# Kernel tuning notes

Measured on AMD Instinct MI355X. Metric: run time of the kernel, lower is better.

Reference implementation:

```python
import jax, jax.numpy as jnp
import numpy as np

HEADS = 8


def setup_inputs() -> dict:
    key = jax.random.key(0)
    ks = jax.random.split(key, 12)
    B, H, W, C = 2, 128, 256, 256
    inner = C  # num_heads * dim_head = 8 * 32

    def p(k, shape):
        return jax.random.normal(k, shape, dtype=jnp.float32) * 0.02

    return {
        "x": jax.random.normal(ks[0], (B, H * W, C), dtype=jnp.float32),
        "Wq_h": p(ks[1], (C, inner)),
        "Wk_h": p(ks[2], (C, inner)),
        "Wv_h": p(ks[3], (C, inner)),
        "Wo_h": p(ks[4], (inner, C)),
        "bo_h": p(ks[5], (C,)),
        "Wq_w": p(ks[6], (C, inner)),
        "Wk_w": p(ks[7], (C, inner)),
        "Wv_w": p(ks[8], (C, inner)),
        "Wo_w": p(ks[9], (inner, C)),
        "bo_w": p(ks[10], (C,)),
        "h": H,
        "w": W,
    }


def reference(x, Wq_h, Wk_h, Wv_h, Wo_h, bo_h, Wq_w, Wk_w, Wv_w, Wo_w, bo_w, h, w):
    b, n, c = x.shape
    heads = HEADS
    d = Wq_h.shape[1] // heads  # dim_head
    scale = d ** -0.5
    xs = x.reshape(b, h, w, c)  # [B,H,W,C]

    def proj(Wm):
        # [B,H,W,heads,d]
        return (xs @ Wm).reshape(b, h, w, heads, d)

    # --- height-axis attention: each column attends across all rows ---
    q, k, v = proj(Wq_h), proj(Wk_h), proj(Wv_h)
    s = jnp.einsum('bxwnd,bywnd->bwnxy', q, k) * scale  # [B,W,heads,H,H]
    a = jax.nn.softmax(s, axis=-1)
    oh = jnp.einsum('bwnxy,bywnd->bxwnd', a, v).reshape(b, h, w, heads * d)
    oh = oh @ Wo_h + bo_h

    # --- width-axis attention: each row attends across all columns ---
    q, k, v = proj(Wq_w), proj(Wk_w), proj(Wv_w)
    s = jnp.einsum('bhxnd,bhynd->bhnxy', q, k) * scale  # [B,H,heads,W,W]
    a = jax.nn.softmax(s, axis=-1)
    ow = jnp.einsum('bhnxy,bhynd->bhxnd', a, v).reshape(b, h, w, heads * d)
    ow = ow @ Wo_w + bo_w

    return (oh + ow).reshape(b, n, c)
```

## Files before the change

kernel.cpp:

```cpp
#include <hip/hip_runtime.h>
#include <hip/hip_bf16.h>
#include <stdint.h>

typedef unsigned short u16;
typedef short bf16x8 __attribute__((ext_vector_type(8)));
typedef float f32x4  __attribute__((ext_vector_type(4)));
typedef float f32x16 __attribute__((ext_vector_type(16)));
typedef unsigned int u32x4 __attribute__((ext_vector_type(4)));

__device__ __forceinline__ u16 f2bf(float f) {
    uint32_t u = __builtin_bit_cast(uint32_t, f);
    u += 0x7fffu + ((u >> 16) & 1u);
    return (u16)(u >> 16);
}

#if __has_builtin(__builtin_amdgcn_exp2f)
#define EXP2(x) __builtin_amdgcn_exp2f(x)
#else
extern "C" __device__ float __ocml_native_exp2_f32(float);
#define EXP2(x) __ocml_native_exp2_f32(x)
#endif

__device__ __forceinline__ void gl_lds16(const u16* g, u16* l) {
    __builtin_amdgcn_global_load_lds(
        (__attribute__((address_space(1))) void*)(g),
        (__attribute__((address_space(3))) void*)(l),
        16, 0, 0);
}

#define MM 65536
#define CC 256

#define QSCALE (1.4426950408889634f * 0.17677669529663687f)

__device__ __forceinline__ int perm_h(int t) {
    return ((t >> 15) << 15) | ((t & 127) << 8) | ((t >> 7) & 255);
}


__global__ void prep_kernel(
    const float* __restrict__ Wq_h, const float* __restrict__ Wk_h, const float* __restrict__ Wv_h,
    const float* __restrict__ Wo_h, const float* __restrict__ bo_h,
    const float* __restrict__ Wq_w, const float* __restrict__ Wk_w, const float* __restrict__ Wv_w,
    const float* __restrict__ Wo_w, const float* __restrict__ bo_w,
    u16* __restrict__ Wh_t, u16* __restrict__ Ww_t,
    u16* __restrict__ Woh_t, u16* __restrict__ Wow_t,
    u16* __restrict__ Wocat, float* __restrict__ bias)
{
    const int tid = blockIdx.x * 256 + threadIdx.x;
    const int nth = gridDim.x * 256;

    for (int i = tid; i < 768 * 256; i += nth) {
        int n = i >> 8, kk = i & 255;
        int which = n >> 8, nn = n & 255;
        const float* Wsh = (which == 0) ? Wq_h : (which == 1) ? Wk_h : Wv_h;
        const float* Wsw = (which == 0) ? Wq_w : (which == 1) ? Wk_w : Wv_w;
        Wh_t[i] = f2bf(Wsh[kk * 256 + nn]);
        Ww_t[i] = f2bf(Wsw[kk * 256 + nn]);
    }
    for (int i = tid; i < 256 * 256; i += nth) {
        int n = i >> 8, k = i & 255;
        Woh_t[i] = f2bf(Wo_h[k * 256 + n]);
        Wow_t[i] = f2bf(Wo_w[k * 256 + n]);
    }
    for (int i = tid; i < 256 * 512; i += nth) {
        int n = i >> 9, k = i & 511;
        float v = (k < 256) ? Wo_h[k * 256 + n] : Wo_w[(k - 256) * 256 + n];
        Wocat[i] = f2bf(v);
    }
    for (int i = tid; i < 256; i += nth) bias[i] = bo_h[i] + bo_w[i];
}

__global__ __launch_bounds__(256) void xcvt_kernel(const float* __restrict__ x, u16* __restrict__ xb)
{
    int i = blockIdx.x * 256 + threadIdx.x;
    const int nth = gridDim.x * 256;
    const int total = MM * 256 / 8;
    for (; i < total; i += nth) {
        const float* ap = x + (size_t)i * 8;
        float4 f0 = *(const float4*)ap;
        float4 f1 = *(const float4*)(ap + 4);
        u16 o[8] = { f2bf(f0.x), f2bf(f0.y), f2bf(f0.z), f2bf(f0.w),
                     f2bf(f1.x), f2bf(f1.y), f2bf(f1.z), f2bf(f1.w) };
        *(int4*)(xb + (size_t)i * 8) = *(const int4*)o;
    }
}

template<int PH>
__global__ __launch_bounds__(512) void gemm_qkv_kernel(
    const u16* __restrict__ xb, const u16* __restrict__ Bt,
    u16* __restrict__ Qb, u16* __restrict__ Kb, u16* __restrict__ Vb)
{
    constexpr int S = PH ? 128 : 256;
    constexpr int L = PH ? 7 : 8;
    const int K = 256;
    __shared__ u16 sh[24576];
    u16* As = sh;
    u16* Bs = sh + 16384;
    const int tid = threadIdx.x;
    const int lane = tid & 63, wave = tid >> 6;
    const int wm = wave >> 1, wn = wave & 1;
    const int l15 = lane & 15, lq = lane >> 4;

    const int id = blockIdx.x;
    const int xcd = id & 7, wq = id >> 3;
    const int mt = xcd * 32 + wq / 6, nt = wq % 6;
    const int m0 = mt * 256, n0 = nt * 128;

    f32x4 acc[4][4];
#pragma unroll
    for (int i = 0; i < 4; i++)
#pragma unroll
        for (int j = 0; j < 4; j++)
#pragma unroll
            for (int t = 0; t < 4; t++) acc[i][j][t] = 0.0f;

    for (int kt = 0; kt < K; kt += 64) {
        __syncthreads();
#pragma unroll
        for (int i = 0; i < 4; i++) {
            int cid = i * 512 + tid;
            int r = cid >> 3, sc = cid & 7;
            int gk = kt + ((sc ^ (r & 7)) << 3);
            int rm = PH ? perm_h(m0 + r) : (m0 + r);
            gl_lds16(xb + (size_t)rm * 256 + gk, As + cid * 8);
        }
#pragma unroll
        for (int i = 0; i < 2; i++) {
            int cid = i * 512 + tid;
            int r = cid >> 3, sc = cid & 7;
            int gk = kt + ((sc ^ (r & 7)) << 3);
            gl_lds16(Bt + (size_t)(n0 + r) * K + gk, Bs + cid * 8);
        }
        __syncthreads();
#pragma unroll
        for (int ks = 0; ks < 2; ks++) {
            bf16x8 af[4], bfr[4];
#pragma unroll
            for (int i = 0; i < 4; i++) {
                int row = wm * 64 + i * 16 + l15;
                int ca  = ks * 4 + lq;
                af[i]  = *(const bf16x8*)(As + row * 64 + ((ca ^ (row & 7)) << 3));
                int nn  = wn * 64 + i * 16 + l15;
                bfr[i] = *(const bf16x8*)(Bs + nn * 64 + ((ca ^ (nn & 7)) << 3));
            }
#pragma unroll
            for (int i = 0; i < 4; i++)
#pragma unroll
                for (int j = 0; j < 4; j++)
                    acc[i][j] = __builtin_amdgcn_mfma_f32_16x16x32_bf16(af[i], bfr[j], acc[i][j], 0, 0, 0);
        }
    }

    const int ln_ = lane & 31, lh_ = lane >> 5;

    if (nt < 4) {
        const float scale = (nt < 2) ? (float)QSCALE : 1.0f;
        u16* dstb = (nt < 2) ? Qb : Kb;
        const int hg = wave & 3;
        const int half = wave >> 2;
        const int head = (nt & 1) * 4 + hg;

#pragma unroll
        for (int p = 0; p < 2; p++) {
            __syncthreads();
            if ((wm >> 1) == p) {
#pragma unroll
                for (int i = 0; i < 4; i++)
#pragma unroll
                    for (int j = 0; j < 4; j++)
#pragma unroll
                        for (int r = 0; r < 4; r++) {
                            int row = (wm & 1) * 64 + i * 16 + lq * 4 + r;
                            int col = wn * 64 + j * 16 + l15;
                            sh[row * 128 + (col ^ ((row & 7) << 3))] = f2bf(acc[i][j][r] * scale);
                        }
            }
            __syncthreads();
            int base = m0 + p * 128;
            int gi = base >> L;
            int seqbase = base & (S - 1);
            u16* dst = dstb + ((size_t)(gi * 8 + head) * S + seqbase) * 32;
#pragma unroll
            for (int qt = 0; qt < 4; qt++) {
                int row  = qt * 32 + ln_;
                int colb = hg * 32 + half * 16 + lh_ * 8;
                int4 v = *(const int4*)(sh + row * 128 + (colb ^ ((row & 7) << 3)));
                *(int4*)(dst + qt * 1024 + half * 512 + lane * 8) = v;
            }
        }
    } else {
        const int hh = wave & 3;
        const int tq = wave >> 2;
        const int head = (nt - 4) * 4 + hh;

#pragma unroll
        for (int p = 0; p < 2; p++) {
            __syncthreads();
            if ((wm >> 1) == p) {
#pragma unroll
                for (int i = 0; i < 4; i++)
#pragma unroll
                    for (int j = 0; j < 4; j++)
#pragma unroll
                        for (int r = 0; r < 4; r++) {
                            int row = (wm & 1) * 64 + i * 16 + lq * 4 + r;
                            int col = wn * 64 + j * 16 + l15;
                            sh[row * 128 + (col ^ ((row & 7) << 3))] = f2bf(acc[i][j][r]);
                        }
            }
            __syncthreads();
            int base = m0 + p * 128;
            int gi = base >> L;
            int seqbase = base & (S - 1);
            u16* dst = Vb + ((size_t)(gi * 8 + head) * S + seqbase) * 32;
#pragma unroll
            for (int tt = 0; tt < 2; tt++) {
                int t = tq * 2 + tt;
#pragma unroll
                for (int half = 0; half < 2; half++) {
                    u16 o[8];
#pragma unroll
                    for (int j = 0; j < 8; j++) {
                        int row = t * 32 + half * 16 + lh_ * 8 + j;
                        int col = hh * 32 + ln_;
                        o[j] = sh[row * 128 + (col ^ ((row & 7) << 3))];
                    }
                    *(int4*)(dst + t * 1024 + half * 512 + lane * 8) = *(const int4*)o;
                }
            }
        }
    }
}

template<int PH>
__global__ __launch_bounds__(512) void gemm_qk_kernel(
    const float* __restrict__ x, const u16* __restrict__ Bt,
    u16* __restrict__ Qb, u16* __restrict__ Kb)
{
    constexpr int S = PH ? 128 : 256;
    constexpr int L = PH ? 7 : 8;
    const int K = 256;
    __shared__ u16 sh[24576];
    u16* As = sh;
    u16* Bs = sh + 16384;
    const int tid = threadIdx.x;
    const int lane = tid & 63, wave = tid >> 6;
    const int wm = wave >> 1, wn = wave & 1;
    const int l15 = lane & 15, lq = lane >> 4;

    const int id = blockIdx.x;
    const int xcd = id & 7, wq = id >> 3;
    const int mt = xcd * 32 + (wq >> 2), nt = wq & 3;
    const int m0 = mt * 256, n0 = nt * 128;

    f32x4 acc[4][4];
#pragma unroll
    for (int i = 0; i < 4; i++)
#pragma unroll
        for (int j = 0; j < 4; j++)
#pragma unroll
            for (int t = 0; t < 4; t++) acc[i][j][t] = 0.0f;

    for (int kt = 0; kt < K; kt += 64) {
        __syncthreads();
#pragma unroll
        for (int i = 0; i < 4; i++) {
            int cid = i * 512 + tid;
            int r = cid >> 3, sc = cid & 7;
            int gk = kt + ((sc ^ (r & 7)) << 3);
            int rm = PH ? perm_h(m0 + r) : (m0 + r);
            const float* ap = x + (size_t)rm * 256 + gk;
            float4 f0 = *(const float4*)ap;
            float4 f1 = *(const float4*)(ap + 4);
            u16 o[8] = { f2bf(f0.x), f2bf(f0.y), f2bf(f0.z), f2bf(f0.w),
                         f2bf(f1.x), f2bf(f1.y), f2bf(f1.z), f2bf(f1.w) };
            *(int4*)(As + (size_t)cid * 8) = *(const int4*)o;
        }
#pragma unroll
        for (int i = 0; i < 2; i++) {
            int cid = i * 512 + tid;
            int r = cid >> 3, sc = cid & 7;
            int gk = kt + ((sc ^ (r & 7)) << 3);
            *(int4*)(Bs + (size_t)cid * 8) = *(const int4*)(Bt + (size_t)(n0 + r) * K + gk);
        }
        __syncthreads();
#pragma unroll
        for (int ks = 0; ks < 2; ks++) {
            bf16x8 af[4], bfr[4];
#pragma unroll
            for (int i = 0; i < 4; i++) {
                int row = wm * 64 + i * 16 + l15;
                int ca  = ks * 4 + lq;
                af[i]  = *(const bf16x8*)(As + row * 64 + ((ca ^ (row & 7)) << 3));
                int nn  = wn * 64 + i * 16 + l15;
                bfr[i] = *(const bf16x8*)(Bs + nn * 64 + ((ca ^ (nn & 7)) << 3));
            }
#pragma unroll
            for (int i = 0; i < 4; i++)
#pragma unroll
                for (int j = 0; j < 4; j++)
                    acc[i][j] = __builtin_amdgcn_mfma_f32_16x16x32_bf16(af[i], bfr[j], acc[i][j], 0, 0, 0);
        }
    }

    const float scale = (nt < 2) ? (float)QSCALE : 1.0f;
    u16* dstb = (nt < 2) ? Qb : Kb;
    const int ln_ = lane & 31, lh_ = lane >> 5;
    const int hg = wave & 3;
    const int half = wave >> 2;
    const int head = (nt & 1) * 4 + hg;

#pragma unroll
    for (int p = 0; p < 2; p++) {
        __syncthreads();
        if ((wm >> 1) == p) {
#pragma unroll
            for (int i = 0; i < 4; i++)
#pragma unroll
                for (int j = 0; j < 4; j++)
#pragma unroll
                    for (int r = 0; r < 4; r++) {
                        int row = (wm & 1) * 64 + i * 16 + lq * 4 + r;
                        int col = wn * 64 + j * 16 + l15;
                        sh[row * 128 + (col ^ ((row & 7) << 3))] = f2bf(acc[i][j][r] * scale);
                    }
        }
        __syncthreads();
        int base = m0 + p * 128;
        int gi = base >> L;
        int seqbase = base & (S - 1);
        u16* dst = dstb + ((size_t)(gi * 8 + head) * S + seqbase) * 32;
#pragma unroll
        for (int qt = 0; qt < 4; qt++) {
            int row  = qt * 32 + ln_;
            int colb = hg * 32 + half * 16 + lh_ * 8;
            int4 v = *(const int4*)(sh + row * 128 + (colb ^ ((row & 7) << 3)));
            *(int4*)(dst + qt * 1024 + half * 512 + lane * 8) = v;
        }
    }
}

template<int PH>
__global__ __launch_bounds__(256) void gemm_vt_kernel(
    const u16* __restrict__ Wt, const float* __restrict__ x, u16* __restrict__ Vb)
{
    constexpr int S = PH ? 128 : 256;
    const int K = 256;
    __shared__ u16 sh[16384];
    u16* As = sh;
    u16* Bs = sh + 8192;
    const int tid = threadIdx.x;
    const int lane = tid & 63, wave = tid >> 6;
    const int wm = wave & 1, wn = wave >> 1;
    const int l15 = lane & 15, lq = lane >> 4;
    const int m0 = blockIdx.y * 128, n0 = blockIdx.x * 128;

    f32x4 acc[4][4];
#pragma unroll
    for (int i = 0; i < 4; i++)
#pragma unroll
        for (int j = 0; j < 4; j++)
#pragma unroll
            for (int t = 0; t < 4; t++) acc[i][j][t] = 0.0f;

    for (int kt = 0; kt < K; kt += 64) {
        __syncthreads();
#pragma unroll
        for (int i = 0; i < 4; i++) {
            int cid = i * 256 + tid;
            int r = cid >> 3, sc = cid & 7;
            int gk = kt + ((sc ^ (r & 7)) << 3);
            *(int4*)(As + (size_t)cid * 8) = *(const int4*)(Wt + (size_t)(m0 + r) * K + gk);
            int cm = PH ? perm_h(n0 + r) : (n0 + r);
            const float* bp = x + (size_t)cm * 256 + gk;
            float4 f0 = *(const float4*)bp;
            float4 f1 = *(const float4*)(bp + 4);
            u16 o[8] = { f2bf(f0.x), f2bf(f0.y), f2bf(f0.z), f2bf(f0.w),
                         f2bf(f1.x), f2bf(f1.y), f2bf(f1.z), f2bf(f1.w) };
            *(int4*)(Bs + (size_t)cid * 8) = *(const int4*)o;
        }
        __syncthreads();
#pragma unroll
        for (int ks = 0; ks < 2; ks++) {
            bf16x8 af[4], bfr[4];
#pragma unroll
            for (int i = 0; i < 4; i++) {
                int row = wm * 64 + i * 16 + l15;
                int ca  = ks * 4 + lq;
                af[i]  = *(const bf16x8*)(As + row * 64 + ((ca ^ (row & 7)) << 3));
                int nn  = wn * 64 + i * 16 + l15;
                bfr[i] = *(const bf16x8*)(Bs + nn * 64 + ((ca ^ (nn & 7)) << 3));
            }
#pragma unroll
            for (int i = 0; i < 4; i++)
#pragma unroll
                for (int j = 0; j < 4; j++)
                    acc[i][j] = __builtin_amdgcn_mfma_f32_16x16x32_bf16(af[i], bfr[j], acc[i][j], 0, 0, 0);
        }
    }

    __syncthreads();
#pragma unroll
    for (int i = 0; i < 4; i++)
#pragma unroll
        for (int j = 0; j < 4; j++)
#pragma unroll
            for (int r = 0; r < 4; r++) {
                int row = wm * 64 + i * 16 + lq * 4 + r;
                int col = wn * 64 + j * 16 + l15;
                sh[row * 128 + (col ^ ((row & 7) << 3))] = f2bf(acc[i][j][r]);
            }
    __syncthreads();

    const int gi = n0 >> (PH ? 7 : 8);
    const int seqbase = n0 & (S - 1);
    const int head = (m0 >> 5) + wave;
    u16* dst = Vb + ((size_t)(gi * 8 + head) * S + seqbase) * 32;
    const int ln_ = lane & 31, lh_ = lane >> 5;
#pragma unroll
    for (int cl = 0; cl < 4; cl++)
#pragma unroll
        for (int half = 0; half < 2; half++) {
            int row  = wave * 32 + ln_;
            int colb = cl * 32 + half * 16 + lh_ * 8;
            int4 v = *(const int4*)(sh + row * 128 + (colb ^ ((row & 7) << 3)));
            *(int4*)(dst + cl * 1024 + half * 512 + lane * 8) = v;
        }
}

__global__ __launch_bounds__(512) void gemm_out_fused_kernel(
    const u16* __restrict__ Ah, const u16* __restrict__ Aw,
    const u16* __restrict__ Bcat, float* __restrict__ Cout, const float* __restrict__ bias)
{
    const int K = 512, N = 256;
    __shared__ u16 sh[24576];
    u16* As = sh;
    u16* Bs = sh + 16384;
    const int tid = threadIdx.x;
    const int lane = tid & 63, wave = tid >> 6;
    const int wm = wave >> 1, wn = wave & 1;
    const int l15 = lane & 15, lq = lane >> 4;

    const int id = blockIdx.x;
    const int xcd = id & 7, wq = id >> 3;
    const int mt = xcd * 32 + (wq >> 1), nt = wq & 1;
    const int m0 = mt * 256, n0 = nt * 128;

    f32x4 acc[4][4];
#pragma unroll
    for (int i = 0; i < 4; i++)
#pragma unroll
        for (int j = 0; j < 4; j++)
#pragma unroll
            for (int t = 0; t < 4; t++) acc[i][j][t] = 0.0f;

    for (int kt = 0; kt < K; kt += 64) {
        __syncthreads();
        const u16* Abase = (kt < 256) ? Ah : Aw;
        int koff = kt & 255;
#pragma unroll
        for (int i = 0; i < 4; i++) {
            int cid = i * 512 + tid;
            int r = cid >> 3, sc = cid & 7;
            int gs = (sc ^ (r & 7)) << 3;
            gl_lds16(Abase + (size_t)(m0 + r) * 256 + koff + gs, As + cid * 8);
        }
#pragma unroll
        for (int i = 0; i < 2; i++) {
            int cid = i * 512 + tid;
            int r = cid >> 3, sc = cid & 7;
            int gs = (sc ^ (r & 7)) << 3;
            gl_lds16(Bcat + (size_t)(n0 + r) * K + kt + gs, Bs + cid * 8);
        }
        __syncthreads();
#pragma unroll
        for (int ks = 0; ks < 2; ks++) {
            bf16x8 af[4], bfr[4];
#pragma unroll
            for (int i = 0; i < 4; i++) {
                int row = wm * 64 + i * 16 + l15;
                int ca  = ks * 4 + lq;
                af[i]  = *(const bf16x8*)(As + row * 64 + ((ca ^ (row & 7)) << 3));
                int nn  = wn * 64 + i * 16 + l15;
                bfr[i] = *(const bf16x8*)(Bs + nn * 64 + ((ca ^ (nn & 7)) << 3));
            }
#pragma unroll
            for (int i = 0; i < 4; i++)
#pragma unroll
                for (int j = 0; j < 4; j++)
                    acc[i][j] = __builtin_amdgcn_mfma_f32_16x16x32_bf16(af[i], bfr[j], acc[i][j], 0, 0, 0);
        }
    }
#pragma unroll
    for (int i = 0; i < 4; i++)
#pragma unroll
        for (int j = 0; j < 4; j++)
#pragma unroll
            for (int r = 0; r < 4; r++) {
                int row = m0 + wm * 64 + i * 16 + lq * 4 + r;
                int col = n0 + wn * 64 + j * 16 + l15;
                Cout[(size_t)row * N + col] = acc[i][j][r] + bias[col];
            }
}

template<int MODE>
__global__ __launch_bounds__(256) void gemm_out_kernel(
    const u16* __restrict__ A16, const u16* __restrict__ Bt,
    float* __restrict__ Cout, const float* __restrict__ bias)
{
    const int K = 256, N = 256;
    __shared__ u16 As[128 * 64];
    __shared__ u16 Bs[128 * 64];
    const int tid = threadIdx.x;
    const int lane = tid & 63, wave = tid >> 6;
    const int wm = wave & 1, wn = wave >> 1;
    const int l15 = lane & 15, lq = lane >> 4;
    const int m0 = blockIdx.y * 128, n0 = blockIdx.x * 128;

    f32x4 acc[4][4];
#pragma unroll
    for (int i = 0; i < 4; i++)
#pragma unroll
        for (int j = 0; j < 4; j++)
#pragma unroll
            for (int t = 0; t < 4; t++) acc[i][j][t] = 0.0f;

    for (int kt = 0; kt < K; kt += 64) {
        __syncthreads();
#pragma unroll
        for (int i = 0; i < 4; i++) {
            int cid = i * 256 + tid;
            int r = cid >> 3, sc = cid & 7;
            int gk = kt + ((sc ^ (r & 7)) << 3);
            *(int4*)(As + (size_t)cid * 8) = *(const int4*)(A16 + (size_t)(m0 + r) * K + gk);
            *(int4*)(Bs + (size_t)cid * 8) = *(const int4*)(Bt + (size_t)(n0 + r) * K + gk);
        }
        __syncthreads();
#pragma unroll
        for (int ks = 0; ks < 2; ks++) {
            bf16x8 af[4], bfr[4];
#pragma unroll
            for (int i = 0; i < 4; i++) {
                int row = wm * 64 + i * 16 + l15;
                int ca  = ks * 4 + lq;
                af[i]  = *(const bf16x8*)(As + row * 64 + ((ca ^ (row & 7)) << 3));
                int nn  = wn * 64 + i * 16 + l15;
                bfr[i] = *(const bf16x8*)(Bs + nn * 64 + ((ca ^ (nn & 7)) << 3));
            }
#pragma unroll
            for (int i = 0; i < 4; i++)
#pragma unroll
                for (int j = 0; j < 4; j++)
                    acc[i][j] = __builtin_amdgcn_mfma_f32_16x16x32_bf16(af[i], bfr[j], acc[i][j], 0, 0, 0);
        }
    }
#pragma unroll
    for (int i = 0; i < 4; i++)
#pragma unroll
        for (int j = 0; j < 4; j++)
#pragma unroll
            for (int r = 0; r < 4; r++) {
                int row = m0 + wm * 64 + i * 16 + lq * 4 + r;
                int col = n0 + wn * 64 + j * 16 + l15;
                size_t idx = (size_t)row * N + col;
                if (MODE == 1) Cout[idx] = acc[i][j][r] + bias[col];
                else           Cout[idx] += acc[i][j][r];
            }
}

template<int S, int PH, int NT>
__global__ __launch_bounds__(NT) void attn_kernel(
    const u16* __restrict__ Qb, const u16* __restrict__ Kb,
    const u16* __restrict__ Vb, u16* __restrict__ att)
{
    constexpr int NC = S / 32;
    const int tid = threadIdx.x;
    const int lane = tid & 63;
    const int wave = tid >> 6;
    const int ln = lane & 31;
    const int lh = lane >> 5;

    const int bid = blockIdx.x;
    const int head = bid & 7;
    const int gi = bid >> 3;
    const int qs = wave * 32;
    const int g = gi * 8 + head;

    const u16* Qg = Qb + (size_t)g * S * 32;
    const u16* Kg = Kb + (size_t)g * S * 32;
    const u16* Vg = Vb + (size_t)g * S * 32;

    const u16* qp = Qg + (qs >> 5) * 1024 + lane * 8;
    bf16x8 bq0 = *(const bf16x8*)qp;
    bf16x8 bq1 = *(const bf16x8*)(qp + 512);

    f32x16 kz;
#pragma unroll
    for (int t = 0; t < 16; t++) kz[t] = 0.0f;
    asm("" : "+v"(kz));

    float rs[4] = {0.0f, 0.0f, 0.0f, 0.0f};
    f32x16 oacc;
#pragma unroll
    for (int t = 0; t < 16; t++) oacc[t] = 0.0f;

    const u16* kp0 = Kg + lane * 8;
    const u16* vp0 = Vg + lane * 8;
    bf16x8 ak0 = *(const bf16x8*)kp0;
    bf16x8 ak1 = *(const bf16x8*)(kp0 + 512);
    bf16x8 bv0 = *(const bf16x8*)vp0;
    bf16x8 bv1 = *(const bf16x8*)(vp0 + 512);

    for (int c = 0; c < NC; c++) {
        f32x16 z = __builtin_amdgcn_mfma_f32_32x32x16_bf16(ak0, bq0, kz, 0, 0, 0);
        z = __builtin_amdgcn_mfma_f32_32x32x16_bf16(ak1, bq1, z, 0, 0, 0);

        int cn = (c + 1 < NC) ? c + 1 : c;
        const u16* kp = kp0 + cn * 1024;
        const u16* vp = vp0 + cn * 1024;
        bf16x8 nk0 = *(const bf16x8*)kp;
        bf16x8 nk1 = *(const bf16x8*)(kp + 512);
        bf16x8 nv0 = *(const bf16x8*)vp;
        bf16x8 nv1 = *(const bf16x8*)(vp + 512);

        asm("" : "+v"(z));
        float p[16];
#pragma unroll
        for (int r = 0; r < 16; r++) { p[r] = EXP2(z[r]); rs[r & 3] += p[r]; }

        unsigned w[8];
#pragma unroll
        for (int t = 0; t < 8; t++) {
            unsigned d;
            asm("v_cvt_pk_bf16_f32 %0, %1, %2" : "=v"(d) : "v"(p[2 * t]), "v"(p[2 * t + 1]));
            w[t] = d;
        }
        auto s0 = __builtin_amdgcn_permlane32_swap(w[0], w[2], false, false);
        auto s1 = __builtin_amdgcn_permlane32_swap(w[1], w[3], false, false);
        auto s2 = __builtin_amdgcn_permlane32_swap(w[4], w[6], false, false);
        auto s3 = __builtin_amdgcn_permlane32_swap(w[5], w[7], false, false);
        u32x4 a0 = { (unsigned)s0[0], (unsigned)s1[0], (unsigned)s0[1], (unsigned)s1[1] };
        u32x4 a1 = { (unsigned)s2[0], (unsigned)s3[0], (unsigned)s2[1], (unsigned)s3[1] };
        bf16x8 pa0 = __builtin_bit_cast(bf16x8, a0);
        bf16x8 pa1 = __builtin_bit_cast(bf16x8, a1);

        oacc = __builtin_amdgcn_mfma_f32_32x32x16_bf16(pa0, bv0, oacc, 0, 0, 0);
        oacc = __builtin_amdgcn_mfma_f32_32x32x16_bf16(pa1, bv1, oacc, 0, 0, 0);

        ak0 = nk0; ak1 = nk1; bv0 = nv0; bv1 = nv1;
    }

    float rsum = (rs[0] + rs[1]) + (rs[2] + rs[3]);
    rsum += __shfl_xor(rsum, 32);
    float inv = 1.0f / rsum;
#pragma unroll
    for (int r = 0; r < 16; r++) {
        int row = (r & 3) + ((r >> 2) << 3) + (lh << 2);
        float is = __shfl(inv, row);
        int seq = qs + row;
        int m = PH ? ((gi >> 8) * 32768 + seq * 256 + (gi & 255))
                   : (gi * 256 + seq);
        att[(size_t)m * 256 + head * 32 + ln] = f2bf(oacc[r] * is);
    }
}

extern "C" void kernel_launch(void* const* d_in, const int* in_sizes, int n_in,
                              void* d_out, int out_size, void* d_ws, size_t ws_size,
                              hipStream_t stream)
{
    (void)in_sizes; (void)n_in; (void)out_size;
    const float* x    = (const float*)d_in[0];
    const float* Wq_h = (const float*)d_in[1];
    const float* Wk_h = (const float*)d_in[2];
    const float* Wv_h = (const float*)d_in[3];
    const float* Wo_h = (const float*)d_in[4];
    const float* bo_h = (const float*)d_in[5];
    const float* Wq_w = (const float*)d_in[6];
    const float* Wk_w = (const float*)d_in[7];
    const float* Wv_w = (const float*)d_in[8];
    const float* Wo_w = (const float*)d_in[9];
    const float* bo_w = (const float*)d_in[10];

    const size_t NB = (size_t)MM * 256;
    u16* Qb   = (u16*)d_ws;
    u16* Kb   = Qb + NB;
    u16* Vb   = Kb + NB;
    u16* attb = Vb + NB;
    u16* xb   = attb + NB;
    const size_t WT = (size_t)2 * 768 * 256 + (size_t)2 * 256 * 256 + (size_t)256 * 512 + 512;
    const bool use_xb = ws_size >= (5 * NB + WT) * sizeof(u16);
    u16* wp = use_xb ? (xb + NB) : xb;
    u16* Wh_t  = wp;
    u16* Ww_t  = Wh_t + 768 * 256;
    u16* Woh_t = Ww_t + 768 * 256;
    u16* Wow_t = Woh_t + 256 * 256;
    u16* Wocat = Wow_t + 256 * 256;
    float* bias = (float*)(Wocat + 256 * 512);

    prep_kernel<<<512, 256, 0, stream>>>(Wq_h, Wk_h, Wv_h, Wo_h, bo_h,
                                         Wq_w, Wk_w, Wv_w, Wo_w, bo_w,
                                         Wh_t, Ww_t, Woh_t, Wow_t, Wocat, bias);
    if (use_xb)
        xcvt_kernel<<<8192, 256, 0, stream>>>(x, xb);

    if (use_xb) {
        gemm_qkv_kernel<1><<<1536, 512, 0, stream>>>(xb, Wh_t, Qb, Kb, Vb);
        attn_kernel<128, 1, 256><<<4096, 256, 0, stream>>>(Qb, Kb, Vb, attb);

        gemm_qkv_kernel<0><<<1536, 512, 0, stream>>>(xb, Ww_t, Qb, Kb, Vb);
        attn_kernel<256, 0, 512><<<2048, 512, 0, stream>>>(Qb, Kb, Vb, xb);

        gemm_out_fused_kernel<<<512, 512, 0, stream>>>(attb, xb, Wocat,
                                                       (float*)d_out, bias);
    } else {
        gemm_qk_kernel<1><<<1024, 512, 0, stream>>>(x, Wh_t, Qb, Kb);
        gemm_vt_kernel<1><<<dim3(512, 2), 256, 0, stream>>>(Wh_t + 512 * 256, x, Vb);
        attn_kernel<128, 1, 256><<<4096, 256, 0, stream>>>(Qb, Kb, Vb, attb);
        gemm_out_kernel<1><<<dim3(2, 512), 256, 0, stream>>>(attb, Woh_t, (float*)d_out, bias);

        gemm_qk_kernel<0><<<1024, 512, 0, stream>>>(x, Ww_t, Qb, Kb);
        gemm_vt_kernel<0><<<dim3(512, 2), 256, 0, stream>>>(Ww_t + 512 * 256, x, Vb);
        attn_kernel<256, 0, 512><<<2048, 512, 0, stream>>>(Qb, Kb, Vb, attb);
        gemm_out_kernel<2><<<dim3(2, 512), 256, 0, stream>>>(attb, Wow_t, (float*)d_out, nullptr);
    }
}
```

Baseline: 337.9 us.

## Merge height and width QKV and attention passes into single launches

Folds the x-to-bf16 conversion into the weight prep kernel. When the workspace is large enough, it also keeps separate Q/K/V buffers for the two axes, so both QKV GEMMs run in one launch and both attention passes run in one launch. This removes launch gaps and tail effects from serial kernels and gives larger grids for better occupancy. In exchange it needs more workspace, and the code falls back to the old path if the workspace is too small.

Measured after the change: 335.7 us. About the same (-0.6%).

```diff
diff --git a/kernel.cpp b/kernel.cpp
--- a/kernel.cpp
+++ b/kernel.cpp
@@ -38,14 +38,15 @@
 }
 
 
-__global__ void prep_kernel(
+__global__ __launch_bounds__(256) void prepx_kernel(
     const float* __restrict__ Wq_h, const float* __restrict__ Wk_h, const float* __restrict__ Wv_h,
     const float* __restrict__ Wo_h, const float* __restrict__ bo_h,
     const float* __restrict__ Wq_w, const float* __restrict__ Wk_w, const float* __restrict__ Wv_w,
     const float* __restrict__ Wo_w, const float* __restrict__ bo_w,
     u16* __restrict__ Wh_t, u16* __restrict__ Ww_t,
     u16* __restrict__ Woh_t, u16* __restrict__ Wow_t,
-    u16* __restrict__ Wocat, float* __restrict__ bias)
+    u16* __restrict__ Wocat, float* __restrict__ bias,
+    const float* __restrict__ x, u16* __restrict__ xb)
 {
     const int tid = blockIdx.x * 256 + threadIdx.x;
     const int nth = gridDim.x * 256;
@@ -69,20 +70,162 @@
         Wocat[i] = f2bf(v);
     }
     for (int i = tid; i < 256; i += nth) bias[i] = bo_h[i] + bo_w[i];
-}
-
-__global__ __launch_bounds__(256) void xcvt_kernel(const float* __restrict__ x, u16* __restrict__ xb)
-{
-    int i = blockIdx.x * 256 + threadIdx.x;
-    const int nth = gridDim.x * 256;
-    const int total = MM * 256 / 8;
-    for (; i < total; i += nth) {
-        const float* ap = x + (size_t)i * 8;
-        float4 f0 = *(const float4*)ap;
-        float4 f1 = *(const float4*)(ap + 4);
-        u16 o[8] = { f2bf(f0.x), f2bf(f0.y), f2bf(f0.z), f2bf(f0.w),
-                     f2bf(f1.x), f2bf(f1.y), f2bf(f1.z), f2bf(f1.w) };
-        *(int4*)(xb + (size_t)i * 8) = *(const int4*)o;
+
+    if (xb) {
+        const int total = MM * 256 / 8;
+        for (int i = tid; i < total; i += nth) {
+            const float* ap = x + (size_t)i * 8;
+            float4 f0 = *(const float4*)ap;
+            float4 f1 = *(const float4*)(ap + 4);
+            u16 o[8] = { f2bf(f0.x), f2bf(f0.y), f2bf(f0.z), f2bf(f0.w),
+                         f2bf(f1.x), f2bf(f1.y), f2bf(f1.z), f2bf(f1.w) };
+            *(int4*)(xb + (size_t)i * 8) = *(const int4*)o;
+        }
+    }
+}
+
+template<int PH>
+__device__ __forceinline__ void qkv_body(u16* sh, int id,
+    const u16* __restrict__ xb, const u16* __restrict__ Bt,
+    u16* __restrict__ Qb, u16* __restrict__ Kb, u16* __restrict__ Vb)
+{
+    constexpr int S = PH ? 128 : 256;
+    constexpr int L = PH ? 7 : 8;
+    const int K = 256;
+    u16* As = sh;
+    u16* Bs = sh + 16384;
+    const int tid = threadIdx.x;
+    const int lane = tid & 63, wave = tid >> 6;
+    const int wm = wave >> 1, wn = wave & 1;
+    const int l15 = lane & 15, lq = lane >> 4;
+
+    const int xcd = id & 7, wq = id >> 3;
+    const int mt = xcd * 32 + wq / 6, nt = wq % 6;
+    const int m0 = mt * 256, n0 = nt * 128;
+
+    f32x4 acc[4][4];
+#pragma unroll
+    for (int i = 0; i < 4; i++)
+#pragma unroll
+        for (int j = 0; j < 4; j++)
+#pragma unroll
+            for (int t = 0; t < 4; t++) acc[i][j][t] = 0.0f;
+
+    for (int kt = 0; kt < K; kt += 64) {
+        __syncthreads();
+#pragma unroll
+        for (int i = 0; i < 4; i++) {
+            int cid = i * 512 + tid;
+            int r = cid >> 3, sc = cid & 7;
+            int gk = kt + ((sc ^ (r & 7)) << 3);
+            int rm = PH ? perm_h(m0 + r) : (m0 + r);
+            gl_lds16(xb + (size_t)rm * 256 + gk, As + cid * 8);
+        }
+#pragma unroll
+        for (int i = 0; i < 2; i++) {
+            int cid = i * 512 + tid;
+            int r = cid >> 3, sc = cid & 7;
+            int gk = kt + ((sc ^ (r & 7)) << 3);
+            gl_lds16(Bt + (size_t)(n0 + r) * K + gk, Bs + cid * 8);
+        }
+        __syncthreads();
+#pragma unroll
+        for (int ks = 0; ks < 2; ks++) {
+            bf16x8 af[4], bfr[4];
+#pragma unroll
+            for (int i = 0; i < 4; i++) {
+                int row = wm * 64 + i * 16 + l15;
+                int ca  = ks * 4 + lq;
+                af[i]  = *(const bf16x8*)(As + row * 64 + ((ca ^ (row & 7)) << 3));
+                int nn  = wn * 64 + i * 16 + l15;
+                bfr[i] = *(const bf16x8*)(Bs + nn * 64 + ((ca ^ (nn & 7)) << 3));
+            }
+#pragma unroll
+            for (int i = 0; i < 4; i++)
+#pragma unroll
+                for (int j = 0; j < 4; j++)
+                    acc[i][j] = __builtin_amdgcn_mfma_f32_16x16x32_bf16(af[i], bfr[j], acc[i][j], 0, 0, 0);
+        }
+    }
+
+    const int ln_ = lane & 31, lh_ = lane >> 5;
+
+    if (nt < 4) {
+        const float scale = (nt < 2) ? (float)QSCALE : 1.0f;
+        u16* dstb = (nt < 2) ? Qb : Kb;
+        const int hg = wave & 3;
+        const int half = wave >> 2;
+        const int head = (nt & 1) * 4 + hg;
+
+#pragma unroll
+        for (int p = 0; p < 2; p++) {
+            __syncthreads();
+            if ((wm >> 1) == p) {
+#pragma unroll
+                for (int i = 0; i < 4; i++)
+#pragma unroll
+                    for (int j = 0; j < 4; j++)
+#pragma unroll
+                        for (int r = 0; r < 4; r++) {
+                            int row = (wm & 1) * 64 + i * 16 + lq * 4 + r;
+                            int col = wn * 64 + j * 16 + l15;
+                            sh[row * 128 + (col ^ ((row & 7) << 3))] = f2bf(acc[i][j][r] * scale);
+                        }
+            }
+            __syncthreads();
+            int base = m0 + p * 128;
+            int gi = base >> L;
+            int seqbase = base & (S - 1);
+            u16* dst = dstb + ((size_t)(gi * 8 + head) * S + seqbase) * 32;
+#pragma unroll
+            for (int qt = 0; qt < 4; qt++) {
+                int row  = qt * 32 + ln_;
+                int colb = hg * 32 + half * 16 + lh_ * 8;
+                int4 v = *(const int4*)(sh + row * 128 + (colb ^ ((row & 7) << 3)));
+                *(int4*)(dst + qt * 1024 + half * 512 + lane * 8) = v;
+            }
+        }
+    } else {
+        const int hh = wave & 3;
+        const int tq = wave >> 2;
+        const int head = (nt - 4) * 4 + hh;
+
+#pragma unroll
+        for (int p = 0; p < 2; p++) {
+            __syncthreads();
+            if ((wm >> 1) == p) {
+#pragma unroll
+                for (int i = 0; i < 4; i++)
+#pragma unroll
+                    for (int j = 0; j < 4; j++)
+#pragma unroll
+                        for (int r = 0; r < 4; r++) {
+                            int row = (wm & 1) * 64 + i * 16 + lq * 4 + r;
+                            int col = wn * 64 + j * 16 + l15;
+                            sh[row * 128 + (col ^ ((row & 7) << 3))] = f2bf(acc[i][j][r]);
+                        }
+            }
+            __syncthreads();
+            int base = m0 + p * 128;
+            int gi = base >> L;
+            int seqbase = base & (S - 1);
+            u16* dst = Vb + ((size_t)(gi * 8 + head) * S + seqbase) * 32;
+#pragma unroll
+            for (int tt = 0; tt < 2; tt++) {
+                int t = tq * 2 + tt;
+#pragma unroll
+                for (int half = 0; half < 2; half++) {
+                    u16 o[8];
+#pragma unroll
+                    for (int j = 0; j < 8; j++) {
+                        int row = t * 32 + half * 16 + lh_ * 8 + j;
+                        int col = hh * 32 + ln_;
+                        o[j] = sh[row * 128 + (col ^ ((row & 7) << 3))];
+                    }
+                    *(int4*)(dst + t * 1024 + half * 512 + lane * 8) = *(const int4*)o;
+                }
+            }
+        }
     }
 }
 
@@ -91,9 +234,151 @@
     const u16* __restrict__ xb, const u16* __restrict__ Bt,
     u16* __restrict__ Qb, u16* __restrict__ Kb, u16* __restrict__ Vb)
 {
-    constexpr int S = PH ? 128 : 256;
-    constexpr int L = PH ? 7 : 8;
-    const int K = 256;
+    __shared__ u16 sh[24576];
+    qkv_body<PH>(sh, blockIdx.x, xb, Bt, Qb, Kb, Vb);
+}
+
+__global__ __launch_bounds__(512) void qkv_both_kernel(
+    const u16* __restrict__ xb,
+    const u16* __restrict__ Wh_t, const u16* __restrict__ Ww_t,
+    u16* __restrict__ Q1, u16* __restrict__ K1, u16* __restrict__ V1,
+    u16* __restrict__ Q2, u16* __restrict__ K2, u16* __restrict__ V2)
+{
+    __shared__ u16 sh[24576];
+    const int bid = blockIdx.x;
+    if (bid < 1536) qkv_body<1>(sh, bid, xb, Wh_t, Q1, K1, V1);
+    else            qkv_body<0>(sh, bid - 1536, xb, Ww_t, Q2, K2, V2);
+}
+
+template<int S, int PH>
+__device__ __forceinline__ void attn_core(int gi, int head, int qs,
+    const u16* __restrict__ Qb, const u16* __restrict__ Kb,
+    const u16* __restrict__ Vb, u16* __restrict__ att)
+{
+    constexpr int NC = S / 32;
+    const int lane = threadIdx.x & 63;
+    const int ln = lane & 31;
+    const int lh = lane >> 5;
+    const int g = gi * 8 + head;
+
+    const u16* Qg = Qb + (size_t)g * S * 32;
+    const u16* Kg = Kb + (size_t)g * S * 32;
+    const u16* Vg = Vb + (size_t)g * S * 32;
+
+    const u16* qp = Qg + (qs >> 5) * 1024 + lane * 8;
+    bf16x8 bq0 = *(const bf16x8*)qp;
+    bf16x8 bq1 = *(const bf16x8*)(qp + 512);
+
+    f32x16 kz;
+#pragma unroll
+    for (int t = 0; t < 16; t++) kz[t] = 0.0f;
+    asm("" : "+v"(kz));
+
+    float rs[4] = {0.0f, 0.0f, 0.0f, 0.0f};
+    f32x16 oacc;
+#pragma unroll
+    for (int t = 0; t < 16; t++) oacc[t] = 0.0f;
+
+    const u16* kp0 = Kg + lane * 8;
+    const u16* vp0 = Vg + lane * 8;
+    bf16x8 ak0 = *(const bf16x8*)kp0;
+    bf16x8 ak1 = *(const bf16x8*)(kp0 + 512);
+    bf16x8 bv0 = *(const bf16x8*)vp0;
+    bf16x8 bv1 = *(const bf16x8*)(vp0 + 512);
+
+    for (int c = 0; c < NC; c++) {
+        f32x16 z = __builtin_amdgcn_mfma_f32_32x32x16_bf16(ak0, bq0, kz, 0, 0, 0);
+        z = __builtin_amdgcn_mfma_f32_32x32x16_bf16(ak1, bq1, z, 0, 0, 0);
+
+        int cn = (c + 1 < NC) ? c + 1 : c;
+        const u16* kp = kp0 + cn * 1024;
+        const u16* vp = vp0 + cn * 1024;
+        bf16x8 nk0 = *(const bf16x8*)kp;
+        bf16x8 nk1 = *(const bf16x8*)(kp + 512);
+        bf16x8 nv0 = *(const bf16x8*)vp;
+        bf16x8 nv1 = *(const bf16x8*)(vp + 512);
+
+        asm("" : "+v"(z));
+        float p[16];
+#pragma unroll
+        for (int r = 0; r < 16; r++) { p[r] = EXP2(z[r]); rs[r & 3] += p[r]; }
+
+        unsigned w[8];
+#pragma unroll
+        for (int t = 0; t < 8; t++) {
+            unsigned d;
+            asm("v_cvt_pk_bf16_f32 %0, %1, %2" : "=v"(d) : "v"(p[2 * t]), "v"(p[2 * t + 1]));
+            w[t] = d;
+        }
+        auto s0 = __builtin_amdgcn_permlane32_swap(w[0], w[2], false, false);
+        auto s1 = __builtin_amdgcn_permlane32_swap(w[1], w[3], false, false);
+        auto s2 = __builtin_amdgcn_permlane32_swap(w[4], w[6], false, false);
+        auto s3 = __builtin_amdgcn_permlane32_swap(w[5], w[7], false, false);
+        u32x4 a0 = { (unsigned)s0[0], (unsigned)s1[0], (unsigned)s0[1], (unsigned)s1[1] };
+        u32x4 a1 = { (unsigned)s2[0], (unsigned)s3[0], (unsigned)s2[1], (unsigned)s3[1] };
+        bf16x8 pa0 = __builtin_bit_cast(bf16x8, a0);
+        bf16x8 pa1 = __builtin_bit_cast(bf16x8, a1);
+
+        oacc = __builtin_amdgcn_mfma_f32_32x32x16_bf16(pa0, bv0, oacc, 0, 0, 0);
+        oacc = __builtin_amdgcn_mfma_f32_32x32x16_bf16(pa1, bv1, oacc, 0, 0, 0);
+
+        ak0 = nk0; ak1 = nk1; bv0 = nv0; bv1 = nv1;
+    }
+
+    float rsum = (rs[0] + rs[1]) + (rs[2] + rs[3]);
+    rsum += __shfl_xor(rsum, 32);
+    float inv = 1.0f / rsum;
+#pragma unroll
+    for (int r = 0; r < 16; r++) {
+        int row = (r & 3) + ((r >> 2) << 3) + (lh << 2);
+        float is = __shfl(inv, row);
+        int seq = qs + row;
+        int m = PH ? ((gi >> 8) * 32768 + seq * 256 + (gi & 255))
+                   : (gi * 256 + seq);
+        att[(size_t)m * 256 + head * 32 + ln] = f2bf(oacc[r] * is);
+    }
+}
+
+template<int S, int PH, int NT>
+__global__ __launch_bounds__(NT) void attn_kernel(
+    const u16* __restrict__ Qb, const u16* __restrict__ Kb,
+    const u16* __restrict__ Vb, u16* __restrict__ att)
+{
+    const int bid = blockIdx.x;
+    const int head = bid & 7;
+    const int gi = bid >> 3;
+    const int qs = (threadIdx.x >> 6) * 32;
+    attn_core<S, PH>(gi, head, qs, Qb, Kb, Vb, att);
+}
+
+__global__ __launch_bounds__(256) void attn_both_kernel(
+    const u16* __restrict__ Q1, const u16* __restrict__ K1, const u16* __restrict__ V1,
+    u16* __restrict__ att1,
+    const u16* __restrict__ Q2, const u16* __restrict__ K2, const u16* __restrict__ V2,
+    u16* __restrict__ att2)
+{
+    const int bid = blockIdx.x;
+    const int wave = threadIdx.x >> 6;
+    if (bid < 4096) {
+        const int head = bid & 7;
+        const int rest = bid >> 3;
+        const int gi = rest & 255;
+        const int qs = ((rest >> 8) << 7) + wave * 32;
+        attn_core<256, 0>(gi, head, qs, Q2, K2, V2, att2);
+    } else {
+        const int b = bid - 4096;
+        const int head = b & 7;
+        const int gi = b >> 3;
+        const int qs = wave * 32;
+        attn_core<128, 1>(gi, head, qs, Q1, K1, V1, att1);
+    }
+}
+
+__global__ __launch_bounds__(512) void gemm_out_fused_kernel(
+    const u16* __restrict__ Ah, const u16* __restrict__ Aw,
+    const u16* __restrict__ Bcat, float* __restrict__ Cout, const float* __restrict__ bias)
+{
+    const int K = 512, N = 256;
     __shared__ u16 sh[24576];
     u16* As = sh;
     u16* Bs = sh + 16384;
@@ -104,7 +389,7 @@
 
     const int id = blockIdx.x;
     const int xcd = id & 7, wq = id >> 3;
-    const int mt = xcd * 32 + wq / 6, nt = wq % 6;
+    const int mt = xcd * 32 + (wq >> 1), nt = wq & 1;
     const int m0 = mt * 256, n0 = nt * 128;
 
     f32x4 acc[4][4];
@@ -117,20 +402,21 @@
 
     for (int kt = 0; kt < K; kt += 64) {
         __syncthreads();
+        const u16* Abase = (kt < 256) ? Ah : Aw;
+        int koff = kt & 255;
 #pragma unroll
         for (int i = 0; i < 4; i++) {
             int cid = i * 512 + tid;
             int r = cid >> 3, sc = cid & 7;
-            int gk = kt + ((sc ^ (r & 7)) << 3);
-            int rm = PH ? perm_h(m0 + r) : (m0 + r);
-            gl_lds16(xb + (size_t)rm * 256 + gk, As + cid * 8);
+            int gs = (sc ^ (r & 7)) << 3;
+            gl_lds16(Abase + (size_t)(m0 + r) * 256 + koff + gs, As + cid * 8);
         }
 #pragma unroll
         for (int i = 0; i < 2; i++) {
             int cid = i * 512 + tid;
             int r = cid >> 3, sc = cid & 7;
-            int gk = kt + ((sc ^ (r & 7)) << 3);
-            gl_lds16(Bt + (size_t)(n0 + r) * K + gk, Bs + cid * 8);
+            int gs = (sc ^ (r & 7)) << 3;
+            gl_lds16(Bcat + (size_t)(n0 + r) * K + kt + gs, Bs + cid * 8);
         }
         __syncthreads();
 #pragma unroll
@@ -151,86 +437,16 @@
                     acc[i][j] = __builtin_amdgcn_mfma_f32_16x16x32_bf16(af[i], bfr[j], acc[i][j], 0, 0, 0);
         }
     }
-
-    const int ln_ = lane & 31, lh_ = lane >> 5;
-
-    if (nt < 4) {
-        const float scale = (nt < 2) ? (float)QSCALE : 1.0f;
-        u16* dstb = (nt < 2) ? Qb : Kb;
-        const int hg = wave & 3;
-        const int half = wave >> 2;
-        const int head = (nt & 1) * 4 + hg;
-
-#pragma unroll
-        for (int p = 0; p < 2; p++) {
-            __syncthreads();
-            if ((wm >> 1) == p) {
-#pragma unroll
-                for (int i = 0; i < 4; i++)
-#pragma unroll
-                    for (int j = 0; j < 4; j++)
-#pragma unroll
-                        for (int r = 0; r < 4; r++) {
-                            int row = (wm & 1) * 64 + i * 16 + lq * 4 + r;
-                            int col = wn * 64 + j * 16 + l15;
-                            sh[row * 128 + (col ^ ((row & 7) << 3))] = f2bf(acc[i][j][r] * scale);
-                        }
-            }
-            __syncthreads();
-            int base = m0 + p * 128;
-            int gi = base >> L;
-            int seqbase = base & (S - 1);
-            u16* dst = dstb + ((size_t)(gi * 8 + head) * S + seqbase) * 32;
-#pragma unroll
-            for (int qt = 0; qt < 4; qt++) {
-                int row  = qt * 32 + ln_;
-                int colb = hg * 32 + half * 16 + lh_ * 8;
-                int4 v = *(const int4*)(sh + row * 128 + (colb ^ ((row & 7) << 3)));
-                *(int4*)(dst + qt * 1024 + half * 512 + lane * 8) = v;
-            }
-        }
-    } else {
-        const int hh = wave & 3;
-        const int tq = wave >> 2;
-        const int head = (nt - 4) * 4 + hh;
-
-#pragma unroll
-        for (int p = 0; p < 2; p++) {
-            __syncthreads();
-            if ((wm >> 1) == p) {
-#pragma unroll
-                for (int i = 0; i < 4; i++)
-#pragma unroll
-                    for (int j = 0; j < 4; j++)
-#pragma unroll
-                        for (int r = 0; r < 4; r++) {
-                            int row = (wm & 1) * 64 + i * 16 + lq * 4 + r;
-                            int col = wn * 64 + j * 16 + l15;
-                            sh[row * 128 + (col ^ ((row & 7) << 3))] = f2bf(acc[i][j][r]);
-                        }
-            }
-            __syncthreads();
-            int base = m0 + p * 128;
-            int gi = base >> L;
-            int seqbase = base & (S - 1);
-            u16* dst = Vb + ((size_t)(gi * 8 + head) * S + seqbase) * 32;
-#pragma unroll
-            for (int tt = 0; tt < 2; tt++) {
-                int t = tq * 2 + tt;
-#pragma unroll
-                for (int half = 0; half < 2; half++) {
-                    u16 o[8];
-#pragma unroll
-                    for (int j = 0; j < 8; j++) {
-                        int row = t * 32 + half * 16 + lh_ * 8 + j;
-                        int col = hh * 32 + ln_;
-                        o[j] = sh[row * 128 + (col ^ ((row & 7) << 3))];
-                    }
-                    *(int4*)(dst + t * 1024 + half * 512 + lane * 8) = *(const int4*)o;
-                }
-            }
-        }
-    }
+#pragma unroll
+    for (int i = 0; i < 4; i++)
+#pragma unroll
+        for (int j = 0; j < 4; j++)
+#pragma unroll
+            for (int r = 0; r < 4; r++) {
+                int row = m0 + wm * 64 + i * 16 + lq * 4 + r;
+                int col = n0 + wn * 64 + j * 16 + l15;
+                Cout[(size_t)row * N + col] = acc[i][j][r] + bias[col];
+            }
 }
 
 template<int PH>
@@ -429,81 +645,6 @@
         }
 }
 
-__global__ __launch_bounds__(512) void gemm_out_fused_kernel(
-    const u16* __restrict__ Ah, const u16* __restrict__ Aw,
-    const u16* __restrict__ Bcat, float* __restrict__ Cout, const float* __restrict__ bias)
-{
-    const int K = 512, N = 256;
-    __shared__ u16 sh[24576];
-    u16* As = sh;
-    u16* Bs = sh + 16384;
-    const int tid = threadIdx.x;
-    const int lane = tid & 63, wave = tid >> 6;
-    const int wm = wave >> 1, wn = wave & 1;
-    const int l15 = lane & 15, lq = lane >> 4;
-
-    const int id = blockIdx.x;
-    const int xcd = id & 7, wq = id >> 3;
-    const int mt = xcd * 32 + (wq >> 1), nt = wq & 1;
-    const int m0 = mt * 256, n0 = nt * 128;
-
-    f32x4 acc[4][4];
-#pragma unroll
-    for (int i = 0; i < 4; i++)
-#pragma unroll
-        for (int j = 0; j < 4; j++)
-#pragma unroll
-            for (int t = 0; t < 4; t++) acc[i][j][t] = 0.0f;
-
-    for (int kt = 0; kt < K; kt += 64) {
-        __syncthreads();
-        const u16* Abase = (kt < 256) ? Ah : Aw;
-        int koff = kt & 255;
-#pragma unroll
-        for (int i = 0; i < 4; i++) {
-            int cid = i * 512 + tid;
-            int r = cid >> 3, sc = cid & 7;
-            int gs = (sc ^ (r & 7)) << 3;
-            gl_lds16(Abase + (size_t)(m0 + r) * 256 + koff + gs, As + cid * 8);
-        }
-#pragma unroll
-        for (int i = 0; i < 2; i++) {
-            int cid = i * 512 + tid;
-            int r = cid >> 3, sc = cid & 7;
-            int gs = (sc ^ (r & 7)) << 3;
-            gl_lds16(Bcat + (size_t)(n0 + r) * K + kt + gs, Bs + cid * 8);
-        }
-        __syncthreads();
-#pragma unroll
-        for (int ks = 0; ks < 2; ks++) {
-            bf16x8 af[4], bfr[4];
-#pragma unroll
-            for (int i = 0; i < 4; i++) {
-                int row = wm * 64 + i * 16 + l15;
-                int ca  = ks * 4 + lq;
-                af[i]  = *(const bf16x8*)(As + row * 64 + ((ca ^ (row & 7)) << 3));
-                int nn  = wn * 64 + i * 16 + l15;
-                bfr[i] = *(const bf16x8*)(Bs + nn * 64 + ((ca ^ (nn & 7)) << 3));
-            }
-#pragma unroll
-            for (int i = 0; i < 4; i++)
-#pragma unroll
-                for (int j = 0; j < 4; j++)
-                    acc[i][j] = __builtin_amdgcn_mfma_f32_16x16x32_bf16(af[i], bfr[j], acc[i][j], 0, 0, 0);
-        }
-    }
-#pragma unroll
-    for (int i = 0; i < 4; i++)
-#pragma unroll
-        for (int j = 0; j < 4; j++)
-#pragma unroll
-            for (int r = 0; r < 4; r++) {
-                int row = m0 + wm * 64 + i * 16 + lq * 4 + r;
-                int col = n0 + wn * 64 + j * 16 + l15;
-                Cout[(size_t)row * N + col] = acc[i][j][r] + bias[col];
-            }
-}
-
 template<int MODE>
 __global__ __launch_bounds__(256) void gemm_out_kernel(
     const u16* __restrict__ A16, const u16* __restrict__ Bt,
@@ -567,102 +708,6 @@
                 if (MODE == 1) Cout[idx] = acc[i][j][r] + bias[col];
                 else           Cout[idx] += acc[i][j][r];
             }
-}
-
-template<int S, int PH, int NT>
-__global__ __launch_bounds__(NT) void attn_kernel(
-    const u16* __restrict__ Qb, const u16* __restrict__ Kb,
-    const u16* __restrict__ Vb, u16* __restrict__ att)
-{
-    constexpr int NC = S / 32;
-    const int tid = threadIdx.x;
-    const int lane = tid & 63;
-    const int wave = tid >> 6;
-    const int ln = lane & 31;
-    const int lh = lane >> 5;
-
-    const int bid = blockIdx.x;
-    const int head = bid & 7;
-    const int gi = bid >> 3;
-    const int qs = wave * 32;
-    const int g = gi * 8 + head;
-
-    const u16* Qg = Qb + (size_t)g * S * 32;
-    const u16* Kg = Kb + (size_t)g * S * 32;
-    const u16* Vg = Vb + (size_t)g * S * 32;
-
-    const u16* qp = Qg + (qs >> 5) * 1024 + lane * 8;
-    bf16x8 bq0 = *(const bf16x8*)qp;
-    bf16x8 bq1 = *(const bf16x8*)(qp + 512);
-
-    f32x16 kz;
-#pragma unroll
-    for (int t = 0; t < 16; t++) kz[t] = 0.0f;
-    asm("" : "+v"(kz));
-
-    float rs[4] = {0.0f, 0.0f, 0.0f, 0.0f};
-    f32x16 oacc;
-#pragma unroll
-    for (int t = 0; t < 16; t++) oacc[t] = 0.0f;
-
-    const u16* kp0 = Kg + lane * 8;
-    const u16* vp0 = Vg + lane * 8;
-    bf16x8 ak0 = *(const bf16x8*)kp0;
-    bf16x8 ak1 = *(const bf16x8*)(kp0 + 512);
-    bf16x8 bv0 = *(const bf16x8*)vp0;
-    bf16x8 bv1 = *(const bf16x8*)(vp0 + 512);
-
-    for (int c = 0; c < NC; c++) {
-        f32x16 z = __builtin_amdgcn_mfma_f32_32x32x16_bf16(ak0, bq0, kz, 0, 0, 0);
-        z = __builtin_amdgcn_mfma_f32_32x32x16_bf16(ak1, bq1, z, 0, 0, 0);
-
-        int cn = (c + 1 < NC) ? c + 1 : c;
-        const u16* kp = kp0 + cn * 1024;
-        const u16* vp = vp0 + cn * 1024;
-        bf16x8 nk0 = *(const bf16x8*)kp;
-        bf16x8 nk1 = *(const bf16x8*)(kp + 512);
-        bf16x8 nv0 = *(const bf16x8*)vp;
-        bf16x8 nv1 = *(const bf16x8*)(vp + 512);
-
-        asm("" : "+v"(z));
-        float p[16];
-#pragma unroll
-        for (int r = 0; r < 16; r++) { p[r] = EXP2(z[r]); rs[r & 3] += p[r]; }
-
-        unsigned w[8];
-#pragma unroll
-        for (int t = 0; t < 8; t++) {
-            unsigned d;
-            asm("v_cvt_pk_bf16_f32 %0, %1, %2" : "=v"(d) : "v"(p[2 * t]), "v"(p[2 * t + 1]));
-            w[t] = d;
-        }
-        auto s0 = __builtin_amdgcn_permlane32_swap(w[0], w[2], false, false);
-        auto s1 = __builtin_amdgcn_permlane32_swap(w[1], w[3], false, false);
-        auto s2 = __builtin_amdgcn_permlane32_swap(w[4], w[6], false, false);
-        auto s3 = __builtin_amdgcn_permlane32_swap(w[5], w[7], false, false);
-        u32x4 a0 = { (unsigned)s0[0], (unsigned)s1[0], (unsigned)s0[1], (unsigned)s1[1] };
-        u32x4 a1 = { (unsigned)s2[0], (unsigned)s3[0], (unsigned)s2[1], (unsigned)s3[1] };
-        bf16x8 pa0 = __builtin_bit_cast(bf16x8, a0);
-        bf16x8 pa1 = __builtin_bit_cast(bf16x8, a1);
-
-        oacc = __builtin_amdgcn_mfma_f32_32x32x16_bf16(pa0, bv0, oacc, 0, 0, 0);
-        oacc = __builtin_amdgcn_mfma_f32_32x32x16_bf16(pa1, bv1, oacc, 0, 0, 0);
-
-        ak0 = nk0; ak1 = nk1; bv0 = nv0; bv1 = nv1;
-    }
-
-    float rsum = (rs[0] + rs[1]) + (rs[2] + rs[3]);
-    rsum += __shfl_xor(rsum, 32);
-    float inv = 1.0f / rsum;
-#pragma unroll
-    for (int r = 0; r < 16; r++) {
-        int row = (r & 3) + ((r >> 2) << 3) + (lh << 2);
-        float is = __shfl(inv, row);
-        int seq = qs + row;
-        int m = PH ? ((gi >> 8) * 32768 + seq * 256 + (gi & 255))
-                   : (gi * 256 + seq);
-        att[(size_t)m * 256 + head * 32 + ln] = f2bf(oacc[r] * is);
-    }
 }
 
 extern "C" void kernel_launch(void* const* d_in, const int* in_sizes, int n_in,
@@ -683,28 +728,49 @@
     const float* bo_w = (const float*)d_in[10];
 
     const size_t NB = (size_t)MM * 256;
-    u16* Qb   = (u16*)d_ws;
-    u16* Kb   = Qb + NB;
-    u16* Vb   = Kb + NB;
-    u16* attb = Vb + NB;
-    u16* xb   = attb + NB;
     const size_t WT = (size_t)2 * 768 * 256 + (size_t)2 * 256 * 256 + (size_t)256 * 512 + 512;
-    const bool use_xb = ws_size >= (5 * NB + WT) * sizeof(u16);
-    u16* wp = use_xb ? (xb + NB) : xb;
-    u16* Wh_t  = wp;
-    u16* Ww_t  = Wh_t + 768 * 256;
-    u16* Woh_t = Ww_t + 768 * 256;
-    u16* Wow_t = Woh_t + 256 * 256;
-    u16* Wocat = Wow_t + 256 * 256;
-    float* bias = (float*)(Wocat + 256 * 512);
-
-    prep_kernel<<<512, 256, 0, stream>>>(Wq_h, Wk_h, Wv_h, Wo_h, bo_h,
-                                         Wq_w, Wk_w, Wv_w, Wo_w, bo_w,
-                                         Wh_t, Ww_t, Woh_t, Wow_t, Wocat, bias);
-    if (use_xb)
-        xcvt_kernel<<<8192, 256, 0, stream>>>(x, xb);
-
-    if (use_xb) {
+    const bool big = ws_size >= (8 * NB + WT) * sizeof(u16);
+    const bool mid = ws_size >= (5 * NB + WT) * sizeof(u16);
+
+    if (big) {
+        u16* xb = (u16*)d_ws;
+        u16* Q1 = xb + NB;  u16* K1 = Q1 + NB;  u16* V1 = K1 + NB;
+        u16* Q2 = V1 + NB;  u16* K2 = Q2 + NB;  u16* V2 = K2 + NB;
+        u16* attb = V2 + NB;
+        u16* Wh_t  = attb + NB;
+        u16* Ww_t  = Wh_t + 768 * 256;
+        u16* Woh_t = Ww_t + 768 * 256;
+        u16* Wow_t = Woh_t + 256 * 256;
+        u16* Wocat = Wow_t + 256 * 256;
+        float* bias = (float*)(Wocat + 256 * 512);
+
+        prepx_kernel<<<8192, 256, 0, stream>>>(Wq_h, Wk_h, Wv_h, Wo_h, bo_h,
+                                               Wq_w, Wk_w, Wv_w, Wo_w, bo_w,
+                                               Wh_t, Ww_t, Woh_t, Wow_t, Wocat, bias,
+                                               x, xb);
+        qkv_both_kernel<<<3072, 512, 0, stream>>>(xb, Wh_t, Ww_t,
+                                                  Q1, K1, V1, Q2, K2, V2);
+        attn_both_kernel<<<8192, 256, 0, stream>>>(Q1, K1, V1, attb,
+                                                   Q2, K2, V2, xb);
+        gemm_out_fused_kernel<<<512, 512, 0, stream>>>(attb, xb, Wocat,
+                                                       (float*)d_out, bias);
+    } else if (mid) {
+        u16* Qb   = (u16*)d_ws;
+        u16* Kb   = Qb + NB;
+        u16* Vb   = Kb + NB;
+        u16* attb = Vb + NB;
+        u16* xb   = attb + NB;
+        u16* Wh_t  = xb + NB;
+        u16* Ww_t  = Wh_t + 768 * 256;
+        u16* Woh_t = Ww_t + 768 * 256;
+        u16* Wow_t = Woh_t + 256 * 256;
+        u16* Wocat = Wow_t + 256 * 256;
+        float* bias = (float*)(Wocat + 256 * 512);
+
+        prepx_kernel<<<8192, 256, 0, stream>>>(Wq_h, Wk_h, Wv_h, Wo_h, bo_h,
+                                               Wq_w, Wk_w, Wv_w, Wo_w, bo_w,
+                                               Wh_t, Ww_t, Woh_t, Wow_t, Wocat, bias,
+                                               x, xb);
         gemm_qkv_kernel<1><<<1536, 512, 0, stream>>>(xb, Wh_t, Qb, Kb, Vb);
         attn_kernel<128, 1, 256><<<4096, 256, 0, stream>>>(Qb, Kb, Vb, attb);
 
@@ -714,6 +780,21 @@
         gemm_out_fused_kernel<<<512, 512, 0, stream>>>(attb, xb, Wocat,
                                                        (float*)d_out, bias);
     } else {
+        u16* Qb   = (u16*)d_ws;
+        u16* Kb   = Qb + NB;
+        u16* Vb   = Kb + NB;
+        u16* attb = Vb + NB;
+        u16* Wh_t  = attb + NB;
+        u16* Ww_t  = Wh_t + 768 * 256;
+        u16* Woh_t = Ww_t + 768 * 256;
+        u16* Wow_t = Woh_t + 256 * 256;
+        u16* Wocat = Wow_t + 256 * 256;
+        float* bias = (float*)(Wocat + 256 * 512);
+
+        prepx_kernel<<<512, 256, 0, stream>>>(Wq_h, Wk_h, Wv_h, Wo_h, bo_h,
+                                              Wq_w, Wk_w, Wv_w, Wo_w, bo_w,
+                                              Wh_t, Ww_t, Woh_t, Wow_t, Wocat, bias,
+                                              x, nullptr);
         gemm_qk_kernel<1><<<1024, 512, 0, stream>>>(x, Wh_t, Qb, Kb);
         gemm_vt_kernel<1><<<dim3(512, 2), 256, 0, stream>>>(Wh_t + 512 * 256, x, Vb);
         attn_kernel<128, 1, 256><<<4096, 256, 0, stream>>>(Qb, Kb, Vb, attb);
```
